# Optimization experiments

Measured on AMD Instinct MI355X. Metric: run time of the kernel, lower is better.

The kernel has to match this reference:

```python
import jax, jax.numpy as jnp
import numpy as np

DMODEL = 1024
N_EXPERTS = 16
EXPERT_SIZE = 256
K = 4


def setup_inputs() -> dict:
    key = jax.random.key(0)
    k1, k2, k3, k4 = jax.random.split(key, 4)
    std_sel = 1.0 / np.sqrt(DMODEL)
    std_val = 1.0 / np.sqrt(N_EXPERTS * EXPERT_SIZE)
    return {
        "x": jax.random.normal(k1, (4, 2048, DMODEL), dtype=jnp.float32),
        "expert_sel": jax.random.normal(k2, (N_EXPERTS, DMODEL), dtype=jnp.float32) * std_sel,
        "keys": jax.random.normal(k3, (N_EXPERTS, DMODEL, EXPERT_SIZE), dtype=jnp.float32) * std_sel,
        "values": jax.random.normal(k4, (N_EXPERTS, EXPERT_SIZE, DMODEL), dtype=jnp.float32) * std_val,
        "route_scale": jnp.ones((1,), dtype=jnp.float32),
    }


def reference(x, expert_sel, keys, values, route_scale):
    # Routing: sigmoid gating, top-k selection (eval mode: no dropout/bias balancing)
    sel_logits = jnp.einsum("btd,ed->bte", x, expert_sel)  # [B,T,E]
    sel_probs = jax.nn.sigmoid(sel_logits)
    _, sel_index = jax.lax.top_k(sel_probs, K)  # [B,T,K]
    sel_val = jnp.take_along_axis(sel_probs, sel_index, axis=-1)  # [B,T,K]
    sel_val = sel_val / jnp.clip(sel_val.sum(-1, keepdims=True), 1e-9)
    sel_val = sel_val * route_scale  # route_scale shape [1] broadcasts
    # Dense all-expert FFN (as in original), then gather top-k and combine
    scores_all = jax.nn.relu(jnp.einsum("btd,edh->bteh", x, keys))  # [B,T,E,H]
    values_all = jnp.einsum("bteh,ehv->btev", scores_all, values)   # [B,T,E,V]
    sel_idx_exp = sel_index[..., None]  # [B,T,K,1]
    selected = jnp.take_along_axis(values_all, sel_idx_exp, axis=2)  # [B,T,K,V]
    out = (selected * sel_val[..., None]).sum(axis=2)  # [B,T,V]
    return out
```

## Files before the change

### kernel.cpp

```cpp
#include <hip/hip_runtime.h>
#include <math.h>


constexpr int NTOK = 8192;
constexpr int DM   = 1024;
constexpr int NE   = 16;
constexpr int EH   = 256;
constexpr int TK   = 4;
constexpr int CAP  = 8192;

typedef __attribute__((ext_vector_type(8))) short short8;
typedef __attribute__((ext_vector_type(4))) float f32x4;

#define MFMA16(a, b, c) __builtin_amdgcn_mfma_f32_16x16x32_bf16(a, b, c, 0, 0, 0)

__device__ __forceinline__ void gload_lds16(const void* g, void* l) {
    __builtin_amdgcn_global_load_lds(
        (const __attribute__((address_space(1))) void*)g,
        (__attribute__((address_space(3))) void*)l, 16, 0, 0);
}

__device__ __forceinline__ unsigned short f2bf(float f) {
    union { float f; unsigned int u; } x; x.f = f;
    unsigned int r = x.u + 0x7fffu + ((x.u >> 16) & 1u);
    return (unsigned short)(r >> 16);
}
__device__ __forceinline__ float bf2f(unsigned short b) {
    union { unsigned int u; float f; } x; x.u = ((unsigned int)b) << 16;
    return x.f;
}

__global__ __launch_bounds__(256) void route_conv_kernel(
    const float* __restrict__ x, const float* __restrict__ esel,
    const float* __restrict__ rscale,
    unsigned short* __restrict__ xb,
    int4* __restrict__ sel4, float* __restrict__ wtk)
{
    __shared__ float Es[NE * DM];
    int tid = threadIdx.x;

    {
        const float4* src = (const float4*)esel;
        float4* dst = (float4*)Es;
        #pragma unroll
        for (int j = 0; j < 16; ++j) dst[tid + j * 256] = src[tid + j * 256];
    }
    __syncthreads();

    int t    = blockIdx.x * 8 + (tid >> 5);
    int l32  = tid & 31;

    float acc[NE];
    #pragma unroll
    for (int e = 0; e < NE; ++e) acc[e] = 0.f;

    const float4* x4 = (const float4*)(x + (size_t)t * DM);
    const float4* E4 = (const float4*)Es;
    #pragma unroll
    for (int i4 = 0; i4 < 8; ++i4) {
        int d4 = i4 * 32 + l32;
        float4 xv = x4[d4];
        ushort4 cb = { f2bf(xv.x), f2bf(xv.y), f2bf(xv.z), f2bf(xv.w) };
        *(ushort4*)(xb + (size_t)t * DM + d4 * 4) = cb;
        #pragma unroll
        for (int e = 0; e < NE; ++e) {
            float4 wv = E4[e * 256 + d4];
            acc[e] = fmaf(xv.x, wv.x, acc[e]);
            acc[e] = fmaf(xv.y, wv.y, acc[e]);
            acc[e] = fmaf(xv.z, wv.z, acc[e]);
            acc[e] = fmaf(xv.w, wv.w, acc[e]);
        }
    }

    #pragma unroll
    for (int off = 16; off; off >>= 1)
        #pragma unroll
        for (int e = 0; e < NE; ++e)
            acc[e] += __shfl_xor(acc[e], off, 32);

    if (l32 == 0) {
        float p[NE];
        #pragma unroll
        for (int e = 0; e < NE; ++e) p[e] = 1.0f / (1.0f + expf(-acc[e]));

        int   sel_e[TK];
        float sel_p[TK];
        float sum = 0.f;
        #pragma unroll
        for (int k = 0; k < TK; ++k) {
            float best = -INFINITY; int be = NE;
            #pragma unroll
            for (int e = 0; e < NE; ++e) {
                bool take = p[e] > best;
                best = take ? p[e] : best;
                be   = take ? e    : be;
            }
            sel_e[k] = be; sel_p[k] = best; sum += best;
            #pragma unroll
            for (int e = 0; e < NE; ++e) p[e] = (e == be) ? -INFINITY : p[e];
        }

        float wsc = rscale[0] / fmaxf(sum, 1e-9f);
        int4 s = { sel_e[0], sel_e[1], sel_e[2], sel_e[3] };
        sel4[t] = s;
        float4 wv = { sel_p[0] * wsc, sel_p[1] * wsc,
                      sel_p[2] * wsc, sel_p[3] * wsc };
        *(float4*)(wtk + t * TK) = wv;
    }
}

__global__ __launch_bounds__(1024) void compact_kernel(
    const int4* __restrict__ sel4, int* __restrict__ counts,
    int* __restrict__ lpk)
{
    __shared__ int wsum[16];
    int e    = blockIdx.x;
    int tid  = threadIdx.x;
    int w    = tid >> 6;
    int lane = tid & 63;

    int base = 0;
    for (int c = 0; c < NTOK; c += 1024) {
        int t = c + tid;
        int4 s = sel4[t];
        int k = -1;
        if      (s.x == e) k = 0;
        else if (s.y == e) k = 1;
        else if (s.z == e) k = 2;
        else if (s.w == e) k = 3;
        unsigned long long m = __ballot(k >= 0);
        int rank = __popcll(m & ((1ull << lane) - 1ull));
        if (lane == 63) wsum[w] = __popcll(m);
        __syncthreads();
        int prefix = 0, total = 0;
        #pragma unroll
        for (int i = 0; i < 16; ++i) {
            int v = wsum[i];
            prefix += (i < w) ? v : 0;
            total  += v;
        }
        if (k >= 0) lpk[e * CAP + base + prefix + rank] = t * TK + k;
        base += total;
        __syncthreads();
    }
    if (tid == 0) counts[e] = base;
}

__global__ void prefix_kernel(const int* __restrict__ counts,
                              int* __restrict__ gbase)
{
    if (threadIdx.x == 0 && blockIdx.x == 0) {
        int s = 0;
        for (int e = 0; e < NE; ++e) {
            gbase[e] = s;
            s += ((counts[e] + 127) >> 7) << 7;
        }
    }
}

__global__ __launch_bounds__(256) void trans_kernel(
    const float* __restrict__ in, unsigned short* __restrict__ outp, int R, int C)
{
    __shared__ float T[32][33];
    int e = blockIdx.z;
    int r0 = blockIdx.y * 32, c0 = blockIdx.x * 32;
    int ri = threadIdx.x >> 3, cq = threadIdx.x & 7;
    float4 v = *(const float4*)(in + ((size_t)e * R + r0 + ri) * C + c0 + cq * 4);
    T[ri][cq * 4 + 0] = v.x; T[ri][cq * 4 + 1] = v.y;
    T[ri][cq * 4 + 2] = v.z; T[ri][cq * 4 + 3] = v.w;
    __syncthreads();
    int ci = threadIdx.x >> 3, rq = threadIdx.x & 7;
    ushort4 o = { f2bf(T[rq * 4 + 0][ci]), f2bf(T[rq * 4 + 1][ci]),
                  f2bf(T[rq * 4 + 2][ci]), f2bf(T[rq * 4 + 3][ci]) };
    *(ushort4*)(outp + ((size_t)e * C + c0 + ci) * R + r0 + rq * 4) = o;
}

__global__ __launch_bounds__(256) void transV_kernel(
    const float* __restrict__ in, unsigned short* __restrict__ outp)
{
    __shared__ float T[64][33];
    int e  = blockIdx.z;
    int c0 = blockIdx.x * 32;
    int r0 = blockIdx.y * 64;
    int tid = threadIdx.x;
    int kin = tid >> 3, cq = tid & 7;
    {
        float4 v0 = *(const float4*)(in + ((size_t)e * EH + r0 + kin) * DM + c0 + cq * 4);
        float4 v1 = *(const float4*)(in + ((size_t)e * EH + r0 + kin + 32) * DM + c0 + cq * 4);
        T[kin][cq * 4 + 0] = v0.x; T[kin][cq * 4 + 1] = v0.y;
        T[kin][cq * 4 + 2] = v0.z; T[kin][cq * 4 + 3] = v0.w;
        T[kin + 32][cq * 4 + 0] = v1.x; T[kin + 32][cq * 4 + 1] = v1.y;
        T[kin + 32][cq * 4 + 2] = v1.z; T[kin + 32][cq * 4 + 3] = v1.w;
    }
    __syncthreads();
    #pragma unroll
    for (int uu = 0; uu < 2; ++uu) {
        int u = tid + uu * 256;
        int d = u >> 4, lm = u & 15;
        ushort4 o = { f2bf(T[lm][d]), f2bf(T[lm + 16][d]),
                      f2bf(T[lm + 32][d]), f2bf(T[lm + 48][d]) };
        *(ushort4*)(outp + (size_t)e * DM * EH + (size_t)(c0 + d) * EH + r0 + lm * 4) = o;
    }
}

__global__ __launch_bounds__(256, 3) void gemm1_kernel(
    const unsigned short* __restrict__ xb,
    const unsigned short* __restrict__ ktb,
    const int* __restrict__ counts, const int* __restrict__ gbase,
    const int* __restrict__ lpk,
    unsigned short* __restrict__ S)
{
    __shared__ __align__(16) char L[33280];
    char* const Ab = L;
    char* const Bb = L + 16384;
    int* const stok = (int*)(L + 32768);

    int tid = threadIdx.x, lane = tid & 63, w = tid >> 6;
    int lm = lane & 15, q = lane >> 4;
    int rw0 = (w >> 1) * 64, cwh = (w & 1);

    int xp = blockIdx.x & 7, j0 = blockIdx.x >> 3;
    int e0 = xp * 2;
    int c0n = counts[e0], c1n = counts[e0 + 1];
    int n0 = (c0n + 127) >> 7, n1 = (c1n + 127) >> 7;
    int ntot = (n0 + n1) * 2;

    for (int jt = j0; jt < ntot; jt += 64) {
        int e, mt, nt, cnt, gb;
        if (jt < n0 * 2) { e = e0;     mt = jt >> 1;  nt = jt & 1;  cnt = c0n; gb = gbase[e0]; }
        else { int j2 = jt - n0 * 2; e = e0 + 1; mt = j2 >> 1; nt = j2 & 1; cnt = c1n; gb = gbase[e0 + 1]; }

        __syncthreads();
        if (tid < 128) {
            int s = mt * 128 + tid;
            stok[tid] = (s < cnt) ? (lpk[e * CAP + s] >> 2) : 0;
        }
        __syncthreads();

        const unsigned short* kte = ktb + (size_t)e * EH * DM + (size_t)(nt * 128) * DM;

        f32x4 zero = {0.f, 0.f, 0.f, 0.f};
        f32x4 acc[4][4];
        #pragma unroll
        for (int mi = 0; mi < 4; ++mi)
            #pragma unroll
            for (int ni = 0; ni < 4; ++ni) acc[mi][ni] = zero;

        for (int ks = 0; ks < 16; ++ks) {
            if (ks) __syncthreads();
            #pragma unroll
            for (int c = 0; c < 4; ++c) {
                int pos  = c * 4096 + w * 1024;
                int row  = (pos >> 7) + (lane >> 3);
                int colb = (lane & 7) * 16;
                int ce   = (colb ^ ((row & 7) << 4)) >> 1;
                gload_lds16(xb + (size_t)stok[row] * DM + ks * 64 + ce, Ab + pos);
                gload_lds16(kte + (size_t)row * DM + ks * 64 + ce, Bb + pos);
            }
            __syncthreads();
            #pragma unroll
            for (int kk = 0; kk < 2; ++kk) {
                short8 a[4], b[4];
                #pragma unroll
                for (int mi = 0; mi < 4; ++mi) {
                    int row = rw0 + mi * 16 + lm;
                    a[mi] = *(const short8*)(Ab + row * 128 +
                             ((kk * 64 + q * 16) ^ ((row & 7) << 4)));
                }
                #pragma unroll
                for (int ni = 0; ni < 4; ++ni) {
                    int row = cwh * 64 + ni * 16 + lm;
                    b[ni] = *(const short8*)(Bb + row * 128 +
                             ((kk * 64 + q * 16) ^ ((row & 7) << 4)));
                }
                __builtin_amdgcn_s_setprio(1);
                #pragma unroll
                for (int mi = 0; mi < 4; ++mi)
                    #pragma unroll
                    for (int ni = 0; ni < 4; ++ni)
                        acc[mi][ni] = MFMA16(a[mi], b[ni], acc[mi][ni]);
                __builtin_amdgcn_s_setprio(0);
            }
        }

        int cb64 = nt * 2 + cwh;
        #pragma unroll
        for (int mi = 0; mi < 4; ++mi)
            #pragma unroll
            for (int r = 0; r < 4; ++r) {
                int gslot = gb + mt * 128 + rw0 + mi * 16 + q * 4 + r;
                unsigned int lo = (unsigned int)f2bf(fmaxf(acc[mi][0][r], 0.f)) |
                                  ((unsigned int)f2bf(fmaxf(acc[mi][1][r], 0.f)) << 16);
                unsigned int hi = (unsigned int)f2bf(fmaxf(acc[mi][2][r], 0.f)) |
                                  ((unsigned int)f2bf(fmaxf(acc[mi][3][r], 0.f)) << 16);
                uint2 pv = { lo, hi };
                *(uint2*)(S + (size_t)gslot * EH + cb64 * 64 + lm * 4) = pv;
            }
    }
}

template<int USE_SCRATCH>
__global__ __launch_bounds__(256, 3) void gemm2_kernel(
    const unsigned short* __restrict__ S,
    const unsigned short* __restrict__ vtb,
    const int* __restrict__ counts, const int* __restrict__ gbase,
    const int* __restrict__ lpk, const float* __restrict__ wtk,
    unsigned short* __restrict__ oscr,
    float* __restrict__ out)
{
    __shared__ __align__(16) char L[34304];
    char* const Ab = L;
    char* const Bb = L + 16384;
    int*   const spk  = (int*)(L + 32768);
    int*   const stok = (int*)(L + 33280);
    float* const sw   = (float*)(L + 33792);

    int tid = threadIdx.x, lane = tid & 63, w = tid >> 6;
    int lm = lane & 15, q = lane >> 4;
    int rw0 = (w >> 1) * 64, cwh = (w & 1);

    int xp = blockIdx.x & 7, j0 = blockIdx.x >> 3;
    int e0 = xp * 2;
    int c0n = counts[e0], c1n = counts[e0 + 1];
    int n0 = (c0n + 127) >> 7, n1 = (c1n + 127) >> 7;
    int ntot = (n0 + n1) * 8;

    for (int jt = j0; jt < ntot; jt += 256) {
        int e, mt, nt, cnt, gb;
        if (jt < n0 * 8) { e = e0;     mt = jt >> 3;  nt = jt & 7;  cnt = c0n; gb = gbase[e0]; }
        else { int j2 = jt - n0 * 8; e = e0 + 1; mt = j2 >> 3; nt = j2 & 7; cnt = c1n; gb = gbase[e0 + 1]; }

        __syncthreads();
        if (tid < 128) {
            int s = mt * 128 + tid;
            if (s < cnt) {
                int pk = lpk[e * CAP + s];
                spk[tid] = pk;
                if (!USE_SCRATCH) { stok[tid] = pk >> 2; sw[tid] = wtk[pk]; }
            } else {
                spk[tid] = NTOK * TK;
                if (!USE_SCRATCH) { stok[tid] = 0; sw[tid] = 0.f; }
            }
        }
        __syncthreads();

        const unsigned short* Se  = S + (size_t)(gb + mt * 128) * EH;
        const unsigned short* vte = vtb + (size_t)e * DM * EH + (size_t)(nt * 128) * EH;

        f32x4 zero = {0.f, 0.f, 0.f, 0.f};
        f32x4 acc[4][4];
        #pragma unroll
        for (int mi = 0; mi < 4; ++mi)
            #pragma unroll
            for (int ni = 0; ni < 4; ++ni) acc[mi][ni] = zero;

        #pragma unroll
        for (int ks = 0; ks < 4; ++ks) {
            if (ks) __syncthreads();
            #pragma unroll
            for (int c = 0; c < 4; ++c) {
                int pos  = c * 4096 + w * 1024;
                int row  = (pos >> 7) + (lane >> 3);
                int colb = (lane & 7) * 16;
                int ce   = (colb ^ ((row & 7) << 4)) >> 1;
                gload_lds16(Se + (size_t)row * EH + ks * 64 + ce, Ab + pos);
                gload_lds16(vte + (size_t)row * EH + ks * 64 + ce, Bb + pos);
            }
            __syncthreads();
            #pragma unroll
            for (int kk = 0; kk < 2; ++kk) {
                short8 a[4], b[4];
                #pragma unroll
                for (int mi = 0; mi < 4; ++mi) {
                    int row = rw0 + mi * 16 + lm;
                    a[mi] = *(const short8*)(Ab + row * 128 +
                             ((kk * 64 + q * 16) ^ ((row & 7) << 4)));
                }
                #pragma unroll
                for (int ni = 0; ni < 4; ++ni) {
                    int row = cwh * 64 + ni * 16 + lm;
                    b[ni] = *(const short8*)(Bb + row * 128 +
                             ((kk * 64 + q * 16) ^ ((row & 7) << 4)));
                }
                __builtin_amdgcn_s_setprio(1);
                #pragma unroll
                for (int mi = 0; mi < 4; ++mi)
                    #pragma unroll
                    for (int ni = 0; ni < 4; ++ni)
                        acc[mi][ni] = MFMA16(a[mi], b[ni], acc[mi][ni]);
                __builtin_amdgcn_s_setprio(0);
            }
        }

        int cb64 = nt * 2 + cwh;
        #pragma unroll
        for (int mi = 0; mi < 4; ++mi)
            #pragma unroll
            for (int r = 0; r < 4; ++r) {
                int slot = rw0 + mi * 16 + q * 4 + r;
                if (USE_SCRATCH) {
                    int pk = spk[slot];
                    unsigned int lo = (unsigned int)f2bf(acc[mi][0][r]) |
                                      ((unsigned int)f2bf(acc[mi][1][r]) << 16);
                    unsigned int hi = (unsigned int)f2bf(acc[mi][2][r]) |
                                      ((unsigned int)f2bf(acc[mi][3][r]) << 16);
                    uint2 pv = { lo, hi };
                    *(uint2*)(oscr + (size_t)pk * DM + cb64 * 64 + lm * 4) = pv;
                } else {
                    #pragma unroll
                    for (int ni = 0; ni < 4; ++ni) {
                        int d = cb64 * 64 + ni * 16 + lm;
                        atomicAdd(out + (size_t)stok[slot] * DM + d,
                                  sw[slot] * acc[mi][ni][r]);
                    }
                }
            }
    }
}

__global__ __launch_bounds__(256) void combine_kernel(
    const unsigned short* __restrict__ oscr, const float* __restrict__ wtk,
    float* __restrict__ out)
{
    int t   = blockIdx.x * 2 + (threadIdx.x >> 7);
    int l   = threadIdx.x & 127;
    int blk = l >> 3;
    int lm2 = l & 7;
    float o[8] = {0.f, 0.f, 0.f, 0.f, 0.f, 0.f, 0.f, 0.f};
    #pragma unroll
    for (int k = 0; k < TK; ++k) {
        float wv = wtk[t * TK + k];
        uint4 qv = *(const uint4*)(oscr + (size_t)(t * TK + k) * DM +
                                   blk * 64 + lm2 * 8);
        unsigned int us[4] = { qv.x, qv.y, qv.z, qv.w };
        #pragma unroll
        for (int j = 0; j < 4; ++j) {
            o[j * 2 + 0] = fmaf(wv, bf2f((unsigned short)(us[j] & 0xffff)), o[j * 2 + 0]);
            o[j * 2 + 1] = fmaf(wv, bf2f((unsigned short)(us[j] >> 16)),    o[j * 2 + 1]);
        }
    }
    float* ob = out + (size_t)t * DM + blk * 64 + 2 * lm2;
    #pragma unroll
    for (int ni = 0; ni < 4; ++ni) {
        float2 f2 = { o[ni], o[ni + 4] };
        *(float2*)(ob + ni * 16) = f2;
    }
}

extern "C" void kernel_launch(void* const* d_in, const int* in_sizes, int n_in,
                              void* d_out, int out_size, void* d_ws, size_t ws_size,
                              hipStream_t stream) {
    const float* x      = (const float*)d_in[0];
    const float* esel   = (const float*)d_in[1];
    const float* keys   = (const float*)d_in[2];
    const float* values = (const float*)d_in[3];
    const float* rscale = (const float*)d_in[4];
    float* out = (float*)d_out;

    char* ws = (char*)d_ws;
    size_t o = 0;
    auto alloc = [&](size_t sz) { size_t r = o; o = (o + sz + 255) & ~(size_t)255; return r; };
    size_t o_counts = alloc(NE * 4);
    size_t o_gbase  = alloc(NE * 4);
    size_t o_lpk    = alloc((size_t)NE * CAP * 4);
    size_t o_sel4   = alloc((size_t)NTOK * 16);
    size_t o_wtk    = alloc((size_t)NTOK * TK * 4);
    size_t o_xb     = alloc((size_t)NTOK * DM * 2);
    size_t o_ktb    = alloc((size_t)NE * EH * DM * 2);
    size_t o_vtb    = alloc((size_t)NE * DM * EH * 2);
    size_t o_S      = alloc(((size_t)NTOK * TK + NE * 128) * EH * 2);
    size_t need_small = o;
    size_t o_oscr   = alloc(((size_t)NTOK * TK + 128) * DM * 2);
    size_t need_full = o;

    int*            counts = (int*)(ws + o_counts);
    int*            gbase  = (int*)(ws + o_gbase);
    int*            lpk    = (int*)(ws + o_lpk);
    int4*           sel4   = (int4*)(ws + o_sel4);
    float*          wtk    = (float*)(ws + o_wtk);
    unsigned short* xb     = (unsigned short*)(ws + o_xb);
    unsigned short* ktb    = (unsigned short*)(ws + o_ktb);
    unsigned short* vtb    = (unsigned short*)(ws + o_vtb);
    unsigned short* Sbuf   = (unsigned short*)(ws + o_S);
    unsigned short* oscr   = (unsigned short*)(ws + o_oscr);

    bool use_scratch = ws_size >= need_full;
    (void)need_small;

    if (!use_scratch)
        hipMemsetAsync(d_out, 0, (size_t)out_size * sizeof(float), stream);

    route_conv_kernel<<<NTOK / 8, 256, 0, stream>>>(x, esel, rscale, xb,
                                                    sel4, wtk);
    compact_kernel<<<NE, 1024, 0, stream>>>(sel4, counts, lpk);
    prefix_kernel<<<1, 64, 0, stream>>>(counts, gbase);
    trans_kernel<<<dim3(EH / 32, DM / 32, NE), 256, 0, stream>>>(keys, ktb, DM, EH);
    transV_kernel<<<dim3(DM / 32, EH / 64, NE), 256, 0, stream>>>(values, vtb);

    gemm1_kernel<<<512, 256, 0, stream>>>(xb, ktb, counts, gbase, lpk, Sbuf);

    if (use_scratch) {
        gemm2_kernel<1><<<2048, 256, 0, stream>>>(Sbuf, vtb, counts, gbase,
                                                  lpk, wtk, oscr, out);
        combine_kernel<<<NTOK / 2, 256, 0, stream>>>(oscr, wtk, out);
    } else {
        gemm2_kernel<0><<<2048, 256, 0, stream>>>(Sbuf, vtb, counts, gbase,
                                                  lpk, wtk, oscr, out);
    }
}
```

Before: 125.8 us.

## Shrink GEMM tiles for more blocks and fold prefix kernel into GEMMs

Both grouped GEMMs switch to smaller output tiles: gemm1 goes from 128x128 to 128x64 and gemm2 from 128x128 to 64x128. Accumulators and LDS shrink, occupancy bounds rise to 4, and grid sizes double. The goal is more parallelism and better wave occupancy on a problem whose per-expert token counts are small. The separate single-thread prefix kernel is dropped, and each GEMM block now computes the expert base offsets from counts itself. The trade-off is less data reuse per tile, so operands are loaded from global/L2 more times.

```diff
diff --git a/kernel.cpp b/kernel.cpp
--- a/kernel.cpp
+++ b/kernel.cpp
@@ -146,18 +146,6 @@
     if (tid == 0) counts[e] = base;
 }
 
-__global__ void prefix_kernel(const int* __restrict__ counts,
-                              int* __restrict__ gbase)
-{
-    if (threadIdx.x == 0 && blockIdx.x == 0) {
-        int s = 0;
-        for (int e = 0; e < NE; ++e) {
-            gbase[e] = s;
-            s += ((counts[e] + 127) >> 7) << 7;
-        }
-    }
-}
-
 __global__ __launch_bounds__(256) void trans_kernel(
     const float* __restrict__ in, unsigned short* __restrict__ outp, int R, int C)
 {
@@ -203,32 +191,33 @@
     }
 }
 
-__global__ __launch_bounds__(256, 3) void gemm1_kernel(
+__global__ __launch_bounds__(256, 4) void gemm1_kernel(
     const unsigned short* __restrict__ xb,
     const unsigned short* __restrict__ ktb,
-    const int* __restrict__ counts, const int* __restrict__ gbase,
-    const int* __restrict__ lpk,
+    const int* __restrict__ counts, const int* __restrict__ lpk,
     unsigned short* __restrict__ S)
 {
-    __shared__ __align__(16) char L[33280];
+    __shared__ __align__(16) char L[25088];
     char* const Ab = L;
     char* const Bb = L + 16384;
-    int* const stok = (int*)(L + 32768);
+    int* const stok = (int*)(L + 24576);
 
     int tid = threadIdx.x, lane = tid & 63, w = tid >> 6;
     int lm = lane & 15, q = lane >> 4;
-    int rw0 = (w >> 1) * 64, cwh = (w & 1);
 
     int xp = blockIdx.x & 7, j0 = blockIdx.x >> 3;
     int e0 = xp * 2;
     int c0n = counts[e0], c1n = counts[e0 + 1];
     int n0 = (c0n + 127) >> 7, n1 = (c1n + 127) >> 7;
-    int ntot = (n0 + n1) * 2;
-
-    for (int jt = j0; jt < ntot; jt += 64) {
+    int ntot = (n0 + n1) * 4;
+    int gb0 = 0;
+    for (int i = 0; i < e0; ++i) gb0 += ((counts[i] + 127) >> 7) << 7;
+    int gb1 = gb0 + (n0 << 7);
+
+    for (int jt = j0; jt < ntot; jt += 128) {
         int e, mt, nt, cnt, gb;
-        if (jt < n0 * 2) { e = e0;     mt = jt >> 1;  nt = jt & 1;  cnt = c0n; gb = gbase[e0]; }
-        else { int j2 = jt - n0 * 2; e = e0 + 1; mt = j2 >> 1; nt = j2 & 1; cnt = c1n; gb = gbase[e0 + 1]; }
+        if (jt < n0 * 4) { e = e0;     mt = jt >> 2;  nt = jt & 3;  cnt = c0n; gb = gb0; }
+        else { int j2 = jt - n0 * 4; e = e0 + 1; mt = j2 >> 2; nt = j2 & 3; cnt = c1n; gb = gb1; }
 
         __syncthreads();
         if (tid < 128) {
@@ -237,12 +226,12 @@
         }
         __syncthreads();
 
-        const unsigned short* kte = ktb + (size_t)e * EH * DM + (size_t)(nt * 128) * DM;
+        const unsigned short* kte = ktb + (size_t)e * EH * DM + (size_t)(nt * 64) * DM;
 
         f32x4 zero = {0.f, 0.f, 0.f, 0.f};
-        f32x4 acc[4][4];
-        #pragma unroll
-        for (int mi = 0; mi < 4; ++mi)
+        f32x4 acc[2][4];
+        #pragma unroll
+        for (int mi = 0; mi < 2; ++mi)
             #pragma unroll
             for (int ni = 0; ni < 4; ++ni) acc[mi][ni] = zero;
 
@@ -250,32 +239,37 @@
             if (ks) __syncthreads();
             #pragma unroll
             for (int c = 0; c < 4; ++c) {
-                int pos  = c * 4096 + w * 1024;
-                int row  = (pos >> 7) + (lane >> 3);
-                int colb = (lane & 7) * 16;
-                int ce   = (colb ^ ((row & 7) << 4)) >> 1;
+                int pos = c * 4096 + w * 1024;
+                int row = (pos >> 7) + (lane >> 3);
+                int ce  = (((lane & 7) * 16) ^ ((row & 7) << 4)) >> 1;
                 gload_lds16(xb + (size_t)stok[row] * DM + ks * 64 + ce, Ab + pos);
+            }
+            #pragma unroll
+            for (int c = 0; c < 2; ++c) {
+                int pos = c * 4096 + w * 1024;
+                int row = (pos >> 7) + (lane >> 3);
+                int ce  = (((lane & 7) * 16) ^ ((row & 7) << 4)) >> 1;
                 gload_lds16(kte + (size_t)row * DM + ks * 64 + ce, Bb + pos);
             }
             __syncthreads();
             #pragma unroll
             for (int kk = 0; kk < 2; ++kk) {
-                short8 a[4], b[4];
+                short8 a[2], b[4];
                 #pragma unroll
-                for (int mi = 0; mi < 4; ++mi) {
-                    int row = rw0 + mi * 16 + lm;
+                for (int mi = 0; mi < 2; ++mi) {
+                    int row = w * 32 + mi * 16 + lm;
                     a[mi] = *(const short8*)(Ab + row * 128 +
                              ((kk * 64 + q * 16) ^ ((row & 7) << 4)));
                 }
                 #pragma unroll
                 for (int ni = 0; ni < 4; ++ni) {
-                    int row = cwh * 64 + ni * 16 + lm;
+                    int row = ni * 16 + lm;
                     b[ni] = *(const short8*)(Bb + row * 128 +
                              ((kk * 64 + q * 16) ^ ((row & 7) << 4)));
                 }
                 __builtin_amdgcn_s_setprio(1);
                 #pragma unroll
-                for (int mi = 0; mi < 4; ++mi)
+                for (int mi = 0; mi < 2; ++mi)
                     #pragma unroll
                     for (int ni = 0; ni < 4; ++ni)
                         acc[mi][ni] = MFMA16(a[mi], b[ni], acc[mi][ni]);
@@ -283,56 +277,58 @@
             }
         }
 
-        int cb64 = nt * 2 + cwh;
-        #pragma unroll
-        for (int mi = 0; mi < 4; ++mi)
+        #pragma unroll
+        for (int mi = 0; mi < 2; ++mi)
             #pragma unroll
             for (int r = 0; r < 4; ++r) {
-                int gslot = gb + mt * 128 + rw0 + mi * 16 + q * 4 + r;
+                int gslot = gb + mt * 128 + w * 32 + mi * 16 + q * 4 + r;
                 unsigned int lo = (unsigned int)f2bf(fmaxf(acc[mi][0][r], 0.f)) |
                                   ((unsigned int)f2bf(fmaxf(acc[mi][1][r], 0.f)) << 16);
                 unsigned int hi = (unsigned int)f2bf(fmaxf(acc[mi][2][r], 0.f)) |
                                   ((unsigned int)f2bf(fmaxf(acc[mi][3][r], 0.f)) << 16);
                 uint2 pv = { lo, hi };
-                *(uint2*)(S + (size_t)gslot * EH + cb64 * 64 + lm * 4) = pv;
+                *(uint2*)(S + (size_t)gslot * EH + nt * 64 + lm * 4) = pv;
             }
     }
 }
 
 template<int USE_SCRATCH>
-__global__ __launch_bounds__(256, 3) void gemm2_kernel(
+__global__ __launch_bounds__(256, 4) void gemm2_kernel(
     const unsigned short* __restrict__ S,
     const unsigned short* __restrict__ vtb,
-    const int* __restrict__ counts, const int* __restrict__ gbase,
-    const int* __restrict__ lpk, const float* __restrict__ wtk,
+    const int* __restrict__ counts, const int* __restrict__ lpk,
+    const float* __restrict__ wtk,
     unsigned short* __restrict__ oscr,
     float* __restrict__ out)
 {
-    __shared__ __align__(16) char L[34304];
+    __shared__ __align__(16) char L[25344];
     char* const Ab = L;
-    char* const Bb = L + 16384;
-    int*   const spk  = (int*)(L + 32768);
-    int*   const stok = (int*)(L + 33280);
-    float* const sw   = (float*)(L + 33792);
+    char* const Bb = L + 8192;
+    int*   const spk  = (int*)(L + 24576);
+    int*   const stok = (int*)(L + 24832);
+    float* const sw   = (float*)(L + 25088);
 
     int tid = threadIdx.x, lane = tid & 63, w = tid >> 6;
     int lm = lane & 15, q = lane >> 4;
-    int rw0 = (w >> 1) * 64, cwh = (w & 1);
+    int wm = w >> 1, wn = w & 1;
 
     int xp = blockIdx.x & 7, j0 = blockIdx.x >> 3;
     int e0 = xp * 2;
     int c0n = counts[e0], c1n = counts[e0 + 1];
-    int n0 = (c0n + 127) >> 7, n1 = (c1n + 127) >> 7;
-    int ntot = (n0 + n1) * 8;
-
-    for (int jt = j0; jt < ntot; jt += 256) {
+    int m0 = (c0n + 63) >> 6, m1 = (c1n + 63) >> 6;
+    int ntot = (m0 + m1) * 8;
+    int gb0 = 0;
+    for (int i = 0; i < e0; ++i) gb0 += ((counts[i] + 127) >> 7) << 7;
+    int gb1 = gb0 + (((c0n + 127) >> 7) << 7);
+
+    for (int jt = j0; jt < ntot; jt += 512) {
         int e, mt, nt, cnt, gb;
-        if (jt < n0 * 8) { e = e0;     mt = jt >> 3;  nt = jt & 7;  cnt = c0n; gb = gbase[e0]; }
-        else { int j2 = jt - n0 * 8; e = e0 + 1; mt = j2 >> 3; nt = j2 & 7; cnt = c1n; gb = gbase[e0 + 1]; }
+        if (jt < m0 * 8) { e = e0;     mt = jt >> 3;  nt = jt & 7;  cnt = c0n; gb = gb0; }
+        else { int j2 = jt - m0 * 8; e = e0 + 1; mt = j2 >> 3; nt = j2 & 7; cnt = c1n; gb = gb1; }
 
         __syncthreads();
-        if (tid < 128) {
-            int s = mt * 128 + tid;
+        if (tid < 64) {
+            int s = mt * 64 + tid;
             if (s < cnt) {
                 int pk = lpk[e * CAP + s];
                 spk[tid] = pk;
@@ -344,13 +340,13 @@
         }
         __syncthreads();
 
-        const unsigned short* Se  = S + (size_t)(gb + mt * 128) * EH;
+        const unsigned short* Se  = S + (size_t)(gb + mt * 64) * EH;
         const unsigned short* vte = vtb + (size_t)e * DM * EH + (size_t)(nt * 128) * EH;
 
         f32x4 zero = {0.f, 0.f, 0.f, 0.f};
-        f32x4 acc[4][4];
-        #pragma unroll
-        for (int mi = 0; mi < 4; ++mi)
+        f32x4 acc[2][4];
+        #pragma unroll
+        for (int mi = 0; mi < 2; ++mi)
             #pragma unroll
             for (int ni = 0; ni < 4; ++ni) acc[mi][ni] = zero;
 
@@ -358,33 +354,38 @@
         for (int ks = 0; ks < 4; ++ks) {
             if (ks) __syncthreads();
             #pragma unroll
+            for (int c = 0; c < 2; ++c) {
+                int pos = c * 4096 + w * 1024;
+                int row = (pos >> 7) + (lane >> 3);
+                int ce  = (((lane & 7) * 16) ^ ((row & 7) << 4)) >> 1;
+                gload_lds16(Se + (size_t)row * EH + ks * 64 + ce, Ab + pos);
+            }
+            #pragma unroll
             for (int c = 0; c < 4; ++c) {
-                int pos  = c * 4096 + w * 1024;
-                int row  = (pos >> 7) + (lane >> 3);
-                int colb = (lane & 7) * 16;
-                int ce   = (colb ^ ((row & 7) << 4)) >> 1;
-                gload_lds16(Se + (size_t)row * EH + ks * 64 + ce, Ab + pos);
+                int pos = c * 4096 + w * 1024;
+                int row = (pos >> 7) + (lane >> 3);
+                int ce  = (((lane & 7) * 16) ^ ((row & 7) << 4)) >> 1;
                 gload_lds16(vte + (size_t)row * EH + ks * 64 + ce, Bb + pos);
             }
             __syncthreads();
             #pragma unroll
             for (int kk = 0; kk < 2; ++kk) {
-                short8 a[4], b[4];
+                short8 a[2], b[4];
                 #pragma unroll
-                for (int mi = 0; mi < 4; ++mi) {
-                    int row = rw0 + mi * 16 + lm;
+                for (int mi = 0; mi < 2; ++mi) {
+                    int row = wm * 32 + mi * 16 + lm;
                     a[mi] = *(const short8*)(Ab + row * 128 +
                              ((kk * 64 + q * 16) ^ ((row & 7) << 4)));
                 }
                 #pragma unroll
                 for (int ni = 0; ni < 4; ++ni) {
-                    int row = cwh * 64 + ni * 16 + lm;
+                    int row = wn * 64 + ni * 16 + lm;
                     b[ni] = *(const short8*)(Bb + row * 128 +
                              ((kk * 64 + q * 16) ^ ((row & 7) << 4)));
                 }
                 __builtin_amdgcn_s_setprio(1);
                 #pragma unroll
-                for (int mi = 0; mi < 4; ++mi)
+                for (int mi = 0; mi < 2; ++mi)
                     #pragma unroll
                     for (int ni = 0; ni < 4; ++ni)
                         acc[mi][ni] = MFMA16(a[mi], b[ni], acc[mi][ni]);
@@ -392,12 +393,12 @@
             }
         }
 
-        int cb64 = nt * 2 + cwh;
-        #pragma unroll
-        for (int mi = 0; mi < 4; ++mi)
+        int cb64 = nt * 2 + wn;
+        #pragma unroll
+        for (int mi = 0; mi < 2; ++mi)
             #pragma unroll
             for (int r = 0; r < 4; ++r) {
-                int slot = rw0 + mi * 16 + q * 4 + r;
+                int slot = wm * 32 + mi * 16 + q * 4 + r;
                 if (USE_SCRATCH) {
                     int pk = spk[slot];
                     unsigned int lo = (unsigned int)f2bf(acc[mi][0][r]) |
@@ -461,7 +462,6 @@
     size_t o = 0;
     auto alloc = [&](size_t sz) { size_t r = o; o = (o + sz + 255) & ~(size_t)255; return r; };
     size_t o_counts = alloc(NE * 4);
-    size_t o_gbase  = alloc(NE * 4);
     size_t o_lpk    = alloc((size_t)NE * CAP * 4);
     size_t o_sel4   = alloc((size_t)NTOK * 16);
     size_t o_wtk    = alloc((size_t)NTOK * TK * 4);
@@ -474,7 +474,6 @@
     size_t need_full = o;
 
     int*            counts = (int*)(ws + o_counts);
-    int*            gbase  = (int*)(ws + o_gbase);
     int*            lpk    = (int*)(ws + o_lpk);
     int4*           sel4   = (int4*)(ws + o_sel4);
     float*          wtk    = (float*)(ws + o_wtk);
@@ -493,18 +492,17 @@
     route_conv_kernel<<<NTOK / 8, 256, 0, stream>>>(x, esel, rscale, xb,
                                                     sel4, wtk);
     compact_kernel<<<NE, 1024, 0, stream>>>(sel4, counts, lpk);
-    prefix_kernel<<<1, 64, 0, stream>>>(counts, gbase);
     trans_kernel<<<dim3(EH / 32, DM / 32, NE), 256, 0, stream>>>(keys, ktb, DM, EH);
     transV_kernel<<<dim3(DM / 32, EH / 64, NE), 256, 0, stream>>>(values, vtb);
 
-    gemm1_kernel<<<512, 256, 0, stream>>>(xb, ktb, counts, gbase, lpk, Sbuf);
+    gemm1_kernel<<<1024, 256, 0, stream>>>(xb, ktb, counts, lpk, Sbuf);
 
     if (use_scratch) {
-        gemm2_kernel<1><<<2048, 256, 0, stream>>>(Sbuf, vtb, counts, gbase,
+        gemm2_kernel<1><<<4096, 256, 0, stream>>>(Sbuf, vtb, counts,
                                                   lpk, wtk, oscr, out);
         combine_kernel<<<NTOK / 2, 256, 0, stream>>>(oscr, wtk, out);
     } else {
-        gemm2_kernel<0><<<2048, 256, 0, stream>>>(Sbuf, vtb, counts, gbase,
+        gemm2_kernel<0><<<4096, 256, 0, stream>>>(Sbuf, vtb, counts,
                                                   lpk, wtk, oscr, out);
     }
 }
```

Result: no change. 123.4 us (-1.9%).
